# Optimization experiments

Hardware: AMD Instinct MI355X
Metric: run time of the kernel (lower is better)

Reference implementation:

```python
import jax, jax.numpy as jnp
import numpy as np

B, N, F_IN, F_OUT, H = 8, 1024, 128, 128, 8
D_K = F_OUT // H
NEG = -1.0e9


def setup_inputs() -> dict:
    key = jax.random.key(0)
    ks = jax.random.split(key, 10)
    X = jax.random.normal(ks[0], (B, N, F_IN), dtype=jnp.float32)
    A = (jax.random.uniform(ks[1], (B, N, N)) < 0.1).astype(jnp.float32)
    A = jnp.maximum(A, jnp.eye(N, dtype=jnp.float32)[None])
    s_in = 1.0 / np.sqrt(F_IN)
    s_out = 1.0 / np.sqrt(F_OUT)
    Wq = jax.random.uniform(ks[2], (F_OUT, F_IN), minval=-s_in, maxval=s_in)
    bq = jax.random.uniform(ks[3], (F_OUT,), minval=-s_in, maxval=s_in)
    Wk = jax.random.uniform(ks[4], (F_OUT, F_IN), minval=-s_in, maxval=s_in)
    bk = jax.random.uniform(ks[5], (F_OUT,), minval=-s_in, maxval=s_in)
    Wv = jax.random.uniform(ks[6], (F_OUT, F_IN), minval=-s_in, maxval=s_in)
    bv = jax.random.uniform(ks[7], (F_OUT,), minval=-s_in, maxval=s_in)
    Wo = jax.random.uniform(ks[8], (F_OUT, F_OUT), minval=-s_out, maxval=s_out)
    bo = jax.random.uniform(ks[9], (F_OUT,), minval=-s_out, maxval=s_out)
    return {"X": X, "A": A, "Wq": Wq, "bq": bq, "Wk": Wk, "bk": bk,
            "Wv": Wv, "bv": bv, "Wo": Wo, "bo": bo}


def reference(X, A, Wq, bq, Wk, bk, Wv, bv, Wo, bo):
    # QKV projections (nn.Linear: x @ W.T + b), split into heads
    Q = (X @ Wq.T + bq).reshape(B, N, H, D_K).transpose(0, 2, 1, 3)  # [B,H,N,d]
    K = (X @ Wk.T + bk).reshape(B, N, H, D_K).transpose(0, 2, 1, 3)
    V = (X @ Wv.T + bv).reshape(B, N, H, D_K).transpose(0, 2, 1, 3)
    scores = jnp.einsum('bhnd,bhmd->bhnm', Q, K) / jnp.sqrt(
        jnp.asarray(D_K, dtype=Q.dtype))
    # adjacency mask: entries with A<=0 set to -1e9 (matches masked_fill)
    scores = jnp.where(A[:, None, :, :] > 0, scores, NEG)
    attn = jax.nn.softmax(scores, axis=-1)  # dropout is identity at eval
    out = jnp.einsum('bhnm,bhmd->bhnd', attn, V)
    out = out.transpose(0, 2, 1, 3).reshape(B, N, H * D_K)
    return out @ Wo.T + bo
```

## Files before the change

kernel.cpp:

```cpp
#include <hip/hip_runtime.h>
#include <hip/hip_bf16.h>


#define BATCH 8
#define NNODE 1024
#define FEAT  128
#define NHEAD 8
#define CHUNKW 96
#define SPADW  100
#define MAXC   192

typedef __attribute__((ext_vector_type(8))) short short8v;
typedef __attribute__((ext_vector_type(4))) float float4v;

__device__ __forceinline__ unsigned short f2bf(float f) {
  union { float f; unsigned u; } c; c.f = f;
  unsigned u = c.u;
  u += 0x7fff + ((u >> 16) & 1);
  return (unsigned short)(u >> 16);
}
__device__ __forceinline__ float bf2f(unsigned short h) {
  union { unsigned u; float f; } c; c.u = ((unsigned)h) << 16;
  return c.f;
}


__global__ __launch_bounds__(256) void prep_kernel(
    const float* __restrict__ A,
    const float* __restrict__ Wq, const float* __restrict__ Wk,
    const float* __restrict__ Wv, const float* __restrict__ Wo,
    unsigned short* __restrict__ Wh, unsigned short* __restrict__ Wl,
    float* __restrict__ WoT,
    unsigned short* __restrict__ AIdx, int* __restrict__ ACnt) {
  __shared__ unsigned short sIdxP[4][MAXC];
  const int bid = blockIdx.x;
  const int t = threadIdx.x;

  if (bid < 2048) {
    const int w = t >> 6;
    const int lane = t & 63;
    const int rowid = bid * 4 + w;
    const float* Arow = A + (size_t)rowid * NNODE;
    const unsigned long long lt = (1ull << lane) - 1ull;
    int cnt = 0;
    #pragma unroll
    for (int r = 0; r < 4; ++r) {
      const float4 av = *(const float4*)&Arow[r * 256 + lane * 4];
      const unsigned long long m0 = __ballot(av.x > 0.f);
      const unsigned long long m1 = __ballot(av.y > 0.f);
      const unsigned long long m2 = __ballot(av.z > 0.f);
      const unsigned long long m3 = __ballot(av.w > 0.f);
      const int c0n = __popcll(m0), c1n = __popcll(m1), c2n = __popcll(m2);
      const int j0 = r * 256 + lane * 4;
      if (av.x > 0.f) sIdxP[w][cnt + __popcll(m0 & lt)] = (unsigned short)j0;
      if (av.y > 0.f) sIdxP[w][cnt + c0n + __popcll(m1 & lt)] = (unsigned short)(j0 + 1);
      if (av.z > 0.f) sIdxP[w][cnt + c0n + c1n + __popcll(m2 & lt)] = (unsigned short)(j0 + 2);
      if (av.w > 0.f) sIdxP[w][cnt + c0n + c1n + c2n + __popcll(m3 & lt)] = (unsigned short)(j0 + 3);
      cnt += c0n + c1n + c2n + __popcll(m3);
    }
    for (int s = lane; s < cnt; s += 64)
      AIdx[(size_t)rowid * MAXC + s] = sIdxP[w][s];
    if (lane == 0) ACnt[rowid] = cnt;
  } else if (bid < 2072) {
    const int wb = bid - 2048;
    const int m = wb >> 3;
    const int p = wb & 7;
    const float* src = (m == 0) ? Wq : (m == 1) ? Wk : Wv;
    const int c = p * 16 + (t >> 4);
    const int k0 = (t & 15) * 8;
    const float4 a = *(const float4*)&src[c * 128 + k0];
    const float4 b = *(const float4*)&src[c * 128 + k0 + 4];
    const float xs[8] = {a.x, a.y, a.z, a.w, b.x, b.y, b.z, b.w};
    short8v h8, l8;
    #pragma unroll
    for (int e = 0; e < 8; ++e) {
      const unsigned short hs = f2bf(xs[e]);
      h8[e] = (short)hs;
      l8[e] = (short)f2bf(xs[e] - bf2f(hs));
    }
    const int ks = k0 >> 5;
    const int kg = (k0 >> 3) & 3;
    const int lanep = (c & 15) + 16 * kg;
    const size_t off = ((((size_t)m * 8 + p) * 4 + ks) * 64 + lanep) * 8;
    *(short8v*)&Wh[off] = h8;
    *(short8v*)&Wl[off] = l8;
  } else {
    const int c0 = (bid - 2072) * 8;
    #pragma unroll
    for (int e = 0; e < 4; ++e) {
      const int idx = t * 4 + e;
      const int cl = idx >> 7;
      const int k = idx & 127;
      WoT[(size_t)k * 128 + c0 + cl] = Wo[(size_t)(c0 + cl) * 128 + k];
    }
  }
}

__global__ __launch_bounds__(256) void qkv_mfma_kernel(
    const float* __restrict__ X,
    const unsigned short* __restrict__ Wh, const unsigned short* __restrict__ Wl,
    const float* __restrict__ bq, const float* __restrict__ bk,
    const float* __restrict__ bv,
    unsigned short* __restrict__ Q, unsigned short* __restrict__ K,
    unsigned short* __restrict__ V) {
  __shared__ unsigned short sXh[4][4][64][8];
  __shared__ unsigned short sXl[4][4][64][8];

  const int t = threadIdx.x;
  const int w = t >> 6;
  const int l = t & 63;
  const int r0 = blockIdx.x * 64;
  const int ty = blockIdx.y;
  const int tz = blockIdx.z;
  const int c0 = ty * 64;
  const float* bias = (tz == 0) ? bq : (tz == 1) ? bk : bv;
  unsigned short* dst = (tz == 0) ? Q : (tz == 1) ? K : V;
  const float scale = (tz == 0) ? 0.25f : 1.0f;

  #pragma unroll
  for (int it = 0; it < 8; ++it) {
    const int idx = t + it * 256;
    const int row = idx >> 5;
    const int kq = (idx & 31) * 4;
    const float4 xv = *(const float4*)&X[(size_t)(r0 + row) * 128 + kq];
    const float xs[4] = {xv.x, xv.y, xv.z, xv.w};
    const int rowgrp = row >> 4;
    const int row16 = row & 15;
    #pragma unroll
    for (int e = 0; e < 4; ++e) {
      const int k = kq + e;
      const unsigned short hs = f2bf(xs[e]);
      const unsigned short ls = f2bf(xs[e] - bf2f(hs));
      const int ks = k >> 5;
      const int lanep = row16 + 16 * ((k >> 3) & 3);
      const int e7 = k & 7;
      sXh[rowgrp][ks][lanep][e7] = hs;
      sXl[rowgrp][ks][lanep][e7] = ls;
    }
  }
  __syncthreads();

  short8v aH[4], aL[4];
  #pragma unroll
  for (int ks = 0; ks < 4; ++ks) {
    aH[ks] = *(const short8v*)&sXh[w][ks][l][0];
    aL[ks] = *(const short8v*)&sXl[w][ks][l][0];
  }

  float4v acc[4] = {};
  const int wtile0 = tz * 8 + ty * 4;
  #pragma unroll
  for (int ks = 0; ks < 4; ++ks) {
    #pragma unroll
    for (int nt = 0; nt < 4; ++nt) {
      const size_t wb = ((((size_t)wtile0 + nt) * 4 + ks) * 64 + l) * 8;
      const short8v bh = *(const short8v*)&Wh[wb];
      const short8v bl = *(const short8v*)&Wl[wb];
      acc[nt] = __builtin_amdgcn_mfma_f32_16x16x32_bf16(aL[ks], bh, acc[nt], 0, 0, 0);
      acc[nt] = __builtin_amdgcn_mfma_f32_16x16x32_bf16(aH[ks], bl, acc[nt], 0, 0, 0);
      acc[nt] = __builtin_amdgcn_mfma_f32_16x16x32_bf16(aH[ks], bh, acc[nt], 0, 0, 0);
    }
  }

  const int row16 = l & 15;
  const int kgrp = l >> 4;
  #pragma unroll
  for (int nt = 0; nt < 4; ++nt) {
    const int col = c0 + nt * 16 + row16;
    const float bcol = bias[col];
    #pragma unroll
    for (int r = 0; r < 4; ++r) {
      const int row = r0 + w * 16 + kgrp * 4 + r;
      dst[(size_t)row * 128 + col] = f2bf((acc[nt][r] + bcol) * scale);
    }
  }
}

__global__ __launch_bounds__(256) void attn_out_kernel(
    const unsigned short* __restrict__ Qb, const unsigned short* __restrict__ Kb,
    const unsigned short* __restrict__ Vb,
    const unsigned short* __restrict__ AIdx, const int* __restrict__ ACnt,
    const float* __restrict__ WoT, const float* __restrict__ bo,
    float* __restrict__ out) {
  __shared__ float sS[4][NHEAD][SPADW];
  __shared__ unsigned short sIdx[4][MAXC];
  __shared__ float sAx[2][2][64];
  __shared__ float sAy[2][2][64];
  __shared__ float sLh[2][2][NHEAD];
  __shared__ float sY[2][FEAT];

  const int t = threadIdx.x;
  const int w = t >> 6;
  const int lane = t & 63;
  const int pw = w >> 1;
  const int half = w & 1;
  const int b = blockIdx.x & 7;
  const int i0 = ((blockIdx.x >> 3) << 1);
  const int i = i0 + pw;
  const size_t bBase = (size_t)b * NNODE;
  const int rowid = (int)(bBase + i);
  const size_t rowQ = (size_t)rowid * FEAT;

  float q0, q1, q2, q3;
  {
    const ushort4 qu = *(const ushort4*)&Qb[rowQ + 4 * (lane & 31)];
    q0 = bf2f(qu.x); q1 = bf2f(qu.y); q2 = bf2f(qu.z); q3 = bf2f(qu.w);
  }

  const int cnt = ACnt[rowid];
  const int mid = (cnt + 1) >> 1;
  const int begin = half ? mid : 0;
  const int cw = (half ? cnt : mid) - begin;
  for (int s = lane; s < cw; s += 64)
    sIdx[w][s] = AIdx[(size_t)rowid * MAXC + begin + s];

  const int side = lane >> 5;
  const int sgrp = (lane & 31) >> 2;
  const int h = lane >> 3;
  float lacc = 0.f;
  float ax = 0.f, ay = 0.f;

  for (int c0 = 0; c0 < cw; c0 += CHUNKW) {
    const int cs = min(cw - c0, CHUNKW);

    for (int p2 = 0; p2 < cs; p2 += 2) {
      const int s = p2 + side;
      const bool valid = s < cs;
      const int j = sIdx[w][valid ? (c0 + s) : c0];
      const ushort4 ku = *(const ushort4*)&Kb[(bBase + j) * FEAT + 4 * (lane & 31)];
      float part = q0 * bf2f(ku.x) + q1 * bf2f(ku.y) +
                   q2 * bf2f(ku.z) + q3 * bf2f(ku.w);
      part += __shfl_xor(part, 1);
      part += __shfl_xor(part, 2);
      if (valid && (lane & 3) == 0) {
        const float p = __expf(part - 8.0f);
        sS[w][sgrp][s] = p;
        lacc += p;
      }
    }

    #pragma unroll 8
    for (int s = 0; s < cs; ++s) {
      const int j = sIdx[w][c0 + s];
      const unsigned vu = *(const unsigned*)&Vb[(bBase + j) * FEAT + 2 * lane];
      const float p = sS[w][h][s];
      ax += p * bf2f((unsigned short)(vu & 0xffff));
      ay += p * bf2f((unsigned short)(vu >> 16));
    }
  }

  const float lhv = __shfl(lacc, 4 * (lane & 7)) +
                    __shfl(lacc, 32 + 4 * (lane & 7));

  sAx[pw][half][lane] = ax;
  sAy[pw][half][lane] = ay;
  if (lane < NHEAD) sLh[pw][half][lane] = lhv;
  __syncthreads();

  if (half == 0) {
    const float axT = sAx[pw][0][lane] + sAx[pw][1][lane];
    const float ayT = sAy[pw][0][lane] + sAy[pw][1][lane];
    const float lT = sLh[pw][0][h] + sLh[pw][1][h];
    sY[pw][2 * lane] = axT / lT;
    sY[pw][2 * lane + 1] = ayT / lT;
  }
  __syncthreads();

  const int row = t >> 7;
  const int c = t & 127;
  const float* Yr = sY[row];
  float acc = bo[c];
  #pragma unroll 16
  for (int k = 0; k < FEAT; ++k)
    acc += Yr[k] * WoT[(size_t)k * 128 + c];
  out[(bBase + i0 + row) * FEAT + c] = acc;
}

extern "C" void kernel_launch(void* const* d_in, const int* in_sizes, int n_in,
                              void* d_out, int out_size, void* d_ws, size_t ws_size,
                              hipStream_t stream) {
  const float* X  = (const float*)d_in[0];
  const float* A  = (const float*)d_in[1];
  const float* Wq = (const float*)d_in[2];
  const float* bq = (const float*)d_in[3];
  const float* Wk = (const float*)d_in[4];
  const float* bk = (const float*)d_in[5];
  const float* Wv = (const float*)d_in[6];
  const float* bv = (const float*)d_in[7];
  const float* Wo = (const float*)d_in[8];
  const float* bo = (const float*)d_in[9];
  float* out = (float*)d_out;

  const size_t mat = (size_t)BATCH * NNODE * FEAT;
  unsigned short* Qd = (unsigned short*)d_ws;
  unsigned short* Kd = Qd + mat;
  unsigned short* Vd = Kd + mat;
  unsigned short* Wh = Vd + mat;
  unsigned short* Wl = Wh + 3 * 16384;
  unsigned short* AIdx = Wl + 3 * 16384;
  int* ACnt = (int*)(AIdx + (size_t)BATCH * NNODE * MAXC);
  float* WoT = (float*)(ACnt + BATCH * NNODE);

  hipLaunchKernelGGL(prep_kernel, dim3(2088), dim3(256), 0, stream,
                     A, Wq, Wk, Wv, Wo, Wh, Wl, WoT, AIdx, ACnt);
  hipLaunchKernelGGL(qkv_mfma_kernel, dim3(128, 2, 3), dim3(256), 0, stream,
                     X, Wh, Wl, bq, bk, bv, Qd, Kd, Vd);
  hipLaunchKernelGGL(attn_out_kernel, dim3(4096), dim3(256), 0, stream,
                     Qd, Kd, Vd, AIdx, ACnt, WoT, bo, out);
}
```

Measured before the change: 151.3 us.

## Merge QKV projection into prep kernel, splitting weights on the fly

The separate QKV MFMA kernel is folded into the prep kernel as an extra range of blocks. Each block now stages raw fp32 X and W tiles in padded LDS and does the bf16 hi/lo split in registers, so the pre-split weight buffers are gone. This removes one kernel launch and the dependency between the weight split and the projection, letting projection blocks overlap with the adjacency-compaction blocks. The cost is that every block repeats the weight split, tiles are smaller (32 rows), and LDS per block grows, which may lower occupancy for the adjacency blocks that share the pool.

```diff
diff --git a/kernel.cpp b/kernel.cpp
--- a/kernel.cpp
+++ b/kernel.cpp
@@ -9,6 +9,7 @@
 #define CHUNKW 96
 #define SPADW  100
 #define MAXC   192
+#define XLDS_STRIDE 132
 
 typedef __attribute__((ext_vector_type(8))) short short8v;
 typedef __attribute__((ext_vector_type(4))) float float4v;
@@ -24,22 +25,105 @@
   return c.f;
 }
 
-
-__global__ __launch_bounds__(256) void prep_kernel(
-    const float* __restrict__ A,
+__device__ __forceinline__ void split8(const float* src, short8v& h8, short8v& l8) {
+  #pragma unroll
+  for (int e = 0; e < 8; ++e) {
+    const float x = src[e];
+    const unsigned short hs = f2bf(x);
+    h8[e] = (short)hs;
+    l8[e] = (short)f2bf(x - bf2f(hs));
+  }
+}
+
+__global__ __launch_bounds__(256) void pre_kernel(
+    const float* __restrict__ X, const float* __restrict__ A,
     const float* __restrict__ Wq, const float* __restrict__ Wk,
     const float* __restrict__ Wv, const float* __restrict__ Wo,
-    unsigned short* __restrict__ Wh, unsigned short* __restrict__ Wl,
+    const float* __restrict__ bq, const float* __restrict__ bk,
+    const float* __restrict__ bv,
+    unsigned short* __restrict__ Q, unsigned short* __restrict__ K,
+    unsigned short* __restrict__ V,
     float* __restrict__ WoT,
     unsigned short* __restrict__ AIdx, int* __restrict__ ACnt) {
-  __shared__ unsigned short sIdxP[4][MAXC];
+  __shared__ float sPool[(32 + 64) * XLDS_STRIDE];
   const int bid = blockIdx.x;
   const int t = threadIdx.x;
 
-  if (bid < 2048) {
+  if (bid < 1536) {
+    float* sX = sPool;
+    float* sW = sPool + 32 * XLDS_STRIDE;
+    const int tz = bid / 512;
+    const int rem = bid - tz * 512;
+    const int ty = rem >> 8;
+    const int rbk = rem & 255;
+    const int r0 = rbk * 32;
+    const int c0 = ty * 64;
+    const float* src = (tz == 0) ? Wq : (tz == 1) ? Wk : Wv;
+    const float* bias = (tz == 0) ? bq : (tz == 1) ? bk : bv;
+    unsigned short* dst = (tz == 0) ? Q : (tz == 1) ? K : V;
+    const float scale = (tz == 0) ? 0.25f : 1.0f;
+
+    #pragma unroll
+    for (int it = 0; it < 4; ++it) {
+      const int idx = t + it * 256;
+      const int row = idx >> 5;
+      const int kq = (idx & 31) * 4;
+      *(float4*)&sX[row * XLDS_STRIDE + kq] =
+          *(const float4*)&X[(size_t)(r0 + row) * FEAT + kq];
+    }
+    #pragma unroll
+    for (int it = 0; it < 8; ++it) {
+      const int idx = t + it * 256;
+      const int c = idx >> 5;
+      const int kq = (idx & 31) * 4;
+      *(float4*)&sW[c * XLDS_STRIDE + kq] =
+          *(const float4*)&src[(size_t)(c0 + c) * FEAT + kq];
+    }
+    __syncthreads();
+
+    const int w = t >> 6;
+    const int l = t & 63;
+    const int rowgrp = w & 1;
+    const int ch = w >> 1;
+    const int row16 = l & 15;
+    const int kgrp = l >> 4;
+
+    short8v aH[4], aL[4];
+    #pragma unroll
+    for (int ks = 0; ks < 4; ++ks) {
+      const int k0 = ks * 32 + kgrp * 8;
+      split8(&sX[(rowgrp * 16 + row16) * XLDS_STRIDE + k0], aH[ks], aL[ks]);
+    }
+
+    float4v acc[2] = {};
+    #pragma unroll
+    for (int ks = 0; ks < 4; ++ks) {
+      const int k0 = ks * 32 + kgrp * 8;
+      #pragma unroll
+      for (int nt = 0; nt < 2; ++nt) {
+        short8v bh, bl;
+        split8(&sW[(ch * 32 + nt * 16 + row16) * XLDS_STRIDE + k0], bh, bl);
+        acc[nt] = __builtin_amdgcn_mfma_f32_16x16x32_bf16(aL[ks], bh, acc[nt], 0, 0, 0);
+        acc[nt] = __builtin_amdgcn_mfma_f32_16x16x32_bf16(aH[ks], bl, acc[nt], 0, 0, 0);
+        acc[nt] = __builtin_amdgcn_mfma_f32_16x16x32_bf16(aH[ks], bh, acc[nt], 0, 0, 0);
+      }
+    }
+
+    #pragma unroll
+    for (int nt = 0; nt < 2; ++nt) {
+      const int col = c0 + ch * 32 + nt * 16 + row16;
+      const float bcol = bias[col];
+      #pragma unroll
+      for (int r = 0; r < 4; ++r) {
+        const int row = r0 + rowgrp * 16 + kgrp * 4 + r;
+        dst[(size_t)row * FEAT + col] = f2bf((acc[nt][r] + bcol) * scale);
+      }
+    }
+  } else if (bid < 3584) {
+    unsigned short* sIdxP = (unsigned short*)sPool;
     const int w = t >> 6;
     const int lane = t & 63;
-    const int rowid = bid * 4 + w;
+    const int rowid = (bid - 1536) * 4 + w;
     const float* Arow = A + (size_t)rowid * NNODE;
     const unsigned long long lt = (1ull << lane) - 1ull;
     int cnt = 0;
@@ -52,126 +136,23 @@
       const unsigned long long m3 = __ballot(av.w > 0.f);
       const int c0n = __popcll(m0), c1n = __popcll(m1), c2n = __popcll(m2);
       const int j0 = r * 256 + lane * 4;
-      if (av.x > 0.f) sIdxP[w][cnt + __popcll(m0 & lt)] = (unsigned short)j0;
-      if (av.y > 0.f) sIdxP[w][cnt + c0n + __popcll(m1 & lt)] = (unsigned short)(j0 + 1);
-      if (av.z > 0.f) sIdxP[w][cnt + c0n + c1n + __popcll(m2 & lt)] = (unsigned short)(j0 + 2);
-      if (av.w > 0.f) sIdxP[w][cnt + c0n + c1n + c2n + __popcll(m3 & lt)] = (unsigned short)(j0 + 3);
+      if (av.x > 0.f) sIdxP[w * MAXC + cnt + __popcll(m0 & lt)] = (unsigned short)j0;
+      if (av.y > 0.f) sIdxP[w * MAXC + cnt + c0n + __popcll(m1 & lt)] = (unsigned short)(j0 + 1);
+      if (av.z > 0.f) sIdxP[w * MAXC + cnt + c0n + c1n + __popcll(m2 & lt)] = (unsigned short)(j0 + 2);
+      if (av.w > 0.f) sIdxP[w * MAXC + cnt + c0n + c1n + c2n + __popcll(m3 & lt)] = (unsigned short)(j0 + 3);
       cnt += c0n + c1n + c2n + __popcll(m3);
     }
     for (int s = lane; s < cnt; s += 64)
-      AIdx[(size_t)rowid * MAXC + s] = sIdxP[w][s];
+      AIdx[(size_t)rowid * MAXC + s] = sIdxP[w * MAXC + s];
     if (lane == 0) ACnt[rowid] = cnt;
-  } else if (bid < 2072) {
-    const int wb = bid - 2048;
-    const int m = wb >> 3;
-    const int p = wb & 7;
-    const float* src = (m == 0) ? Wq : (m == 1) ? Wk : Wv;
-    const int c = p * 16 + (t >> 4);
-    const int k0 = (t & 15) * 8;
-    const float4 a = *(const float4*)&src[c * 128 + k0];
-    const float4 b = *(const float4*)&src[c * 128 + k0 + 4];
-    const float xs[8] = {a.x, a.y, a.z, a.w, b.x, b.y, b.z, b.w};
-    short8v h8, l8;
-    #pragma unroll
-    for (int e = 0; e < 8; ++e) {
-      const unsigned short hs = f2bf(xs[e]);
-      h8[e] = (short)hs;
-      l8[e] = (short)f2bf(xs[e] - bf2f(hs));
-    }
-    const int ks = k0 >> 5;
-    const int kg = (k0 >> 3) & 3;
-    const int lanep = (c & 15) + 16 * kg;
-    const size_t off = ((((size_t)m * 8 + p) * 4 + ks) * 64 + lanep) * 8;
-    *(short8v*)&Wh[off] = h8;
-    *(short8v*)&Wl[off] = l8;
   } else {
-    const int c0 = (bid - 2072) * 8;
+    const int c0 = (bid - 3584) * 8;
     #pragma unroll
     for (int e = 0; e < 4; ++e) {
       const int idx = t * 4 + e;
       const int cl = idx >> 7;
       const int k = idx & 127;
-      WoT[(size_t)k * 128 + c0 + cl] = Wo[(size_t)(c0 + cl) * 128 + k];
-    }
-  }
-}
-
-__global__ __launch_bounds__(256) void qkv_mfma_kernel(
-    const float* __restrict__ X,
-    const unsigned short* __restrict__ Wh, const unsigned short* __restrict__ Wl,
-    const float* __restrict__ bq, const float* __restrict__ bk,
-    const float* __restrict__ bv,
-    unsigned short* __restrict__ Q, unsigned short* __restrict__ K,
-    unsigned short* __restrict__ V) {
-  __shared__ unsigned short sXh[4][4][64][8];
-  __shared__ unsigned short sXl[4][4][64][8];
-
-  const int t = threadIdx.x;
-  const int w = t >> 6;
-  const int l = t & 63;
-  const int r0 = blockIdx.x * 64;
-  const int ty = blockIdx.y;
-  const int tz = blockIdx.z;
-  const int c0 = ty * 64;
-  const float* bias = (tz == 0) ? bq : (tz == 1) ? bk : bv;
-  unsigned short* dst = (tz == 0) ? Q : (tz == 1) ? K : V;
-  const float scale = (tz == 0) ? 0.25f : 1.0f;
-
-  #pragma unroll
-  for (int it = 0; it < 8; ++it) {
-    const int idx = t + it * 256;
-    const int row = idx >> 5;
-    const int kq = (idx & 31) * 4;
-    const float4 xv = *(const float4*)&X[(size_t)(r0 + row) * 128 + kq];
-    const float xs[4] = {xv.x, xv.y, xv.z, xv.w};
-    const int rowgrp = row >> 4;
-    const int row16 = row & 15;
-    #pragma unroll
-    for (int e = 0; e < 4; ++e) {
-      const int k = kq + e;
-      const unsigned short hs = f2bf(xs[e]);
-      const unsigned short ls = f2bf(xs[e] - bf2f(hs));
-      const int ks = k >> 5;
-      const int lanep = row16 + 16 * ((k >> 3) & 3);
-      const int e7 = k & 7;
-      sXh[rowgrp][ks][lanep][e7] = hs;
-      sXl[rowgrp][ks][lanep][e7] = ls;
-    }
-  }
-  __syncthreads();
-
-  short8v aH[4], aL[4];
-  #pragma unroll
-  for (int ks = 0; ks < 4; ++ks) {
-    aH[ks] = *(const short8v*)&sXh[w][ks][l][0];
-    aL[ks] = *(const short8v*)&sXl[w][ks][l][0];
-  }
-
-  float4v acc[4] = {};
-  const int wtile0 = tz * 8 + ty * 4;
-  #pragma unroll
-  for (int ks = 0; ks < 4; ++ks) {
-    #pragma unroll
-    for (int nt = 0; nt < 4; ++nt) {
-      const size_t wb = ((((size_t)wtile0 + nt) * 4 + ks) * 64 + l) * 8;
-      const short8v bh = *(const short8v*)&Wh[wb];
-      const short8v bl = *(const short8v*)&Wl[wb];
-      acc[nt] = __builtin_amdgcn_mfma_f32_16x16x32_bf16(aL[ks], bh, acc[nt], 0, 0, 0);
-      acc[nt] = __builtin_amdgcn_mfma_f32_16x16x32_bf16(aH[ks], bl, acc[nt], 0, 0, 0);
-      acc[nt] = __builtin_amdgcn_mfma_f32_16x16x32_bf16(aH[ks], bh, acc[nt], 0, 0, 0);
-    }
-  }
-
-  const int row16 = l & 15;
-  const int kgrp = l >> 4;
-  #pragma unroll
-  for (int nt = 0; nt < 4; ++nt) {
-    const int col = c0 + nt * 16 + row16;
-    const float bcol = bias[col];
-    #pragma unroll
-    for (int r = 0; r < 4; ++r) {
-      const int row = r0 + w * 16 + kgrp * 4 + r;
-      dst[(size_t)row * 128 + col] = f2bf((acc[nt][r] + bcol) * scale);
+      WoT[(size_t)k * FEAT + c0 + cl] = Wo[(size_t)(c0 + cl) * FEAT + k];
     }
   }
 }
@@ -295,16 +276,13 @@
   unsigned short* Qd = (unsigned short*)d_ws;
   unsigned short* Kd = Qd + mat;
   unsigned short* Vd = Kd + mat;
-  unsigned short* Wh = Vd + mat;
-  unsigned short* Wl = Wh + 3 * 16384;
-  unsigned short* AIdx = Wl + 3 * 16384;
+  unsigned short* AIdx = Vd + mat;
   int* ACnt = (int*)(AIdx + (size_t)BATCH * NNODE * MAXC);
   float* WoT = (float*)(ACnt + BATCH * NNODE);
 
-  hipLaunchKernelGGL(prep_kernel, dim3(2088), dim3(256), 0, stream,
-                     A, Wq, Wk, Wv, Wo, Wh, Wl, WoT, AIdx, ACnt);
-  hipLaunchKernelGGL(qkv_mfma_kernel, dim3(128, 2, 3), dim3(256), 0, stream,
-                     X, Wh, Wl, bq, bk, bv, Qd, Kd, Vd);
+  hipLaunchKernelGGL(pre_kernel, dim3(3600), dim3(256), 0, stream,
+                     X, A, Wq, Wk, Wv, Wo, bq, bk, bv,
+                     Qd, Kd, Vd, WoT, AIdx, ACnt);
   hipLaunchKernelGGL(attn_out_kernel, dim3(4096), dim3(256), 0, stream,
                      Qd, Kd, Vd, AIdx, ACnt, WoT, bo, out);
 }
```

Measured after the change: 152.2 us. Within noise of the previous version (+0.6%).
